# Kernel optimization log

Measured on AMD Instinct MI355X. Metric: run time of the kernel, lower is better.

Reference implementation:

```python
import jax, jax.numpy as jnp
import numpy as np

N = 50000      # nodes
E = 800000     # edges (avg degree 16)
D = 128        # hidden dim
L = 3          # message-passing layers
NU = 1         # DRew nu -> delay = max(k - nu, 0)


def setup_inputs() -> dict:
    key = jax.random.key(0)
    ks = jax.random.split(key, 6)
    x = jax.random.normal(ks[0], (N, D), dtype=jnp.float32)
    edge_index = jax.random.randint(ks[1], (2, E), 0, N)          # [2, E] (src, dst)
    edge_attr = jax.random.randint(ks[2], (E,), 1, L + 1)          # edge types in {1..L}
    scale = 1.0 / np.sqrt(D).astype(np.float32)
    Ws = jax.random.normal(ks[3], (L, D, D), dtype=jnp.float32) * scale       # mlp_s per layer
    bs = jnp.zeros((L, D), dtype=jnp.float32)
    Wk = jax.random.normal(ks[4], (L, L, D, D), dtype=jnp.float32) * scale    # mlp_k, padded; layer t uses k=1..t+1
    bk = jnp.zeros((L, L, D), dtype=jnp.float32)
    eps = jnp.zeros((L,), dtype=jnp.float32)
    return dict(x=x, edge_index=edge_index, edge_attr=edge_attr,
                Ws=Ws, bs=bs, Wk=Wk, bk=bk, eps=eps)


def reference(x, edge_index, edge_attr, Ws, bs, Wk, bk, eps):
    src, dst = edge_index[0], edge_index[1]
    xs = [x]
    for t in range(L):
        xt = xs[-1]
        # out = (1 + eps) * mlp_s(x)
        out = (1.0 + eps[t]) * jax.nn.relu(xt @ Ws[t] + bs[t])
        for k in range(1, t + 2):
            delay = max(k - NU, 0)
            x_src = xs[t - delay]                       # delayed node features
            mask = (edge_attr == k).astype(xt.dtype)    # edge-type mask (replaces boolean column select)
            msg = x_src[src] * mask[:, None]            # gather + mask: [E, D]
            agg = jax.ops.segment_sum(msg, dst, num_segments=N)  # scatter-add per destination
            out = out + jax.nn.relu(agg @ Wk[t, k - 1] + bk[t, k - 1])  # mlp_k(k)
        # gin_nn_post is an empty Sequential -> identity; then F.relu; then residual
        h = jax.nn.relu(out)
        xs.append(xt + h)
    return xs[-1]
```

## Files before the change

### kernel.cpp

```cpp
#include <hip/hip_runtime.h>
#include <hip/hip_bf16.h>


#define NODES 50000
#define EDGES 800000
#define DIM   128
#define ND    ((long)NODES * DIM)
#define NB3   (3 * NODES)
#define NPART 4
#define PSIZE (NODES / NPART)
#define NROWP 50048
#define NBLKS ((NB3 + 255) / 256)
#define NCELL 96
#define SORTN (NCELL * NBLKS)

typedef __attribute__((ext_vector_type(8))) short  bf16x8;
typedef __attribute__((ext_vector_type(4))) float  f32x4;

#define LDS_STRIDE 136

__global__ __launch_bounds__(256) void init_kernel(
    const float* __restrict__ x, const float* __restrict__ Ws,
    const float* __restrict__ Wk, __hip_bfloat16* __restrict__ xb0,
    __hip_bfloat16* __restrict__ xb1, __hip_bfloat16* __restrict__ xb2,
    __hip_bfloat16* __restrict__ WT, int* __restrict__ cursor) {
  int b = blockIdx.x, tid = threadIdx.x;
  long i = (long)b * 256 + tid;
  if (i < ND / 4) {
    float4 v = ((const float4*)x)[i];
    union { __hip_bfloat16 h[4]; uint2 u; } pk;
    pk.h[0] = __float2bfloat16(v.x); pk.h[1] = __float2bfloat16(v.y);
    pk.h[2] = __float2bfloat16(v.z); pk.h[3] = __float2bfloat16(v.w);
    ((uint2*)xb0)[i] = pk.u;
  }
  if (b < 12) {
    const float* src = (b < 3) ? (Ws + (long)b * 16384) : (Wk + (long)(b - 3) * 16384);
    __hip_bfloat16* dst = WT + (long)b * 16384;
    for (int idx = tid; idx < 16384; idx += 256) {
      int k = idx >> 7, n = idx & 127;
      dst[n * 128 + k] = __float2bfloat16(src[idx]);
    }
  }
  if (b >= 12 && b < 12 + NBLKS) {
    int g = (b - 12) * 256 + tid;
    if (g < NB3) cursor[g] = 0;
  }
  if (b == 599 && tid < DIM) {
    xb0[(long)NODES * DIM + tid] = __float2bfloat16(0.f);
    xb1[(long)NODES * DIM + tid] = __float2bfloat16(0.f);
    xb2[(long)NODES * DIM + tid] = __float2bfloat16(0.f);
  }
}

__global__ __launch_bounds__(256) void hist_kernel(
    const int* __restrict__ ei, const int* __restrict__ attr,
    int* __restrict__ counts, int E) {
  int e = blockIdx.x * 256 + threadIdx.x;
  if (e >= E) return;
  atomicAdd(&counts[ei[E + e] * 3 + (attr[e] - 1)], 1);
}

__global__ __launch_bounds__(256) void scan_a_kernel(
    const int* __restrict__ counts, int* __restrict__ partial,
    int* __restrict__ blocksums, int n) {
  __shared__ int tmp[256];
  int gid = blockIdx.x * 256 + threadIdx.x;
  int v = (gid < n) ? ((counts[gid] + 3) & ~3) : 0;
  tmp[threadIdx.x] = v;
  __syncthreads();
  for (int off = 1; off < 256; off <<= 1) {
    int t = (threadIdx.x >= off) ? tmp[threadIdx.x - off] : 0;
    __syncthreads();
    tmp[threadIdx.x] += t;
    __syncthreads();
  }
  if (gid < n) partial[gid] = tmp[threadIdx.x] - v;
  if (threadIdx.x == 255) blocksums[blockIdx.x] = tmp[255];
}

__global__ __launch_bounds__(256) void scan_b_kernel(int* __restrict__ bs, int nb) {
  __shared__ int tmp[256];
  __shared__ int carry;
  if (threadIdx.x == 0) carry = 0;
  __syncthreads();
  for (int base = 0; base < nb; base += 256) {
    int gid = base + threadIdx.x;
    int v = (gid < nb) ? bs[gid] : 0;
    tmp[threadIdx.x] = v;
    __syncthreads();
    for (int off = 1; off < 256; off <<= 1) {
      int t = (threadIdx.x >= off) ? tmp[threadIdx.x - off] : 0;
      __syncthreads();
      tmp[threadIdx.x] += t;
      __syncthreads();
    }
    if (gid < nb) bs[gid] = tmp[threadIdx.x] - v + carry;
    __syncthreads();
    if (threadIdx.x == 0) carry += tmp[255];
    __syncthreads();
  }
}

__global__ __launch_bounds__(256) void scanc_bhist_kernel(
    int* __restrict__ rowptr, int* __restrict__ cursor,
    const int* __restrict__ bs, int* __restrict__ csr,
    int* __restrict__ G, int n) {
  __shared__ int h[NCELL];
  if (threadIdx.x < NCELL) h[threadIdx.x] = 0;
  __syncthreads();
  int gid = blockIdx.x * 256 + threadIdx.x;
  if (gid < n) {
    int cnt = cursor[gid];
    int pcnt = (cnt + 3) & ~3;
    int val = rowptr[gid] + bs[blockIdx.x];
    rowptr[gid] = val;
    cursor[gid] = val;
    for (int i = cnt; i < pcnt; ++i) csr[val + i] = NODES;
    if (gid == n - 1) rowptr[n] = val + pcnt;
    int c = pcnt >> 2; if (c > 31) c = 31;
    int km1 = gid - (gid / 3) * 3;
    atomicAdd(&h[km1 * 32 + (31 - c)], 1);
  }
  __syncthreads();
  if (threadIdx.x < NCELL) G[threadIdx.x * NBLKS + blockIdx.x] = h[threadIdx.x];
}

__global__ __launch_bounds__(256) void fill_kernel(
    const int* __restrict__ ei, const int* __restrict__ attr,
    int* __restrict__ cursor, int* __restrict__ csr_src, int E) {
  int p = blockIdx.x & (NPART - 1);
  int chunk = blockIdx.x >> 2;
  int e = chunk * 256 + threadIdx.x;
  if (e >= E) return;
  int d = ei[E + e];
  int lo = p * PSIZE;
  if (d < lo || d >= lo + PSIZE) return;
  int pos = atomicAdd(&cursor[d * 3 + (attr[e] - 1)], 1);
  csr_src[pos] = ei[e];
}

__global__ __launch_bounds__(256) void fscan_a_kernel(
    const int* __restrict__ in, int* __restrict__ partial,
    int* __restrict__ blocksums, int n) {
  __shared__ int tmp[256];
  int gid = blockIdx.x * 256 + threadIdx.x;
  int v = (gid < n) ? in[gid] : 0;
  tmp[threadIdx.x] = v;
  __syncthreads();
  for (int off = 1; off < 256; off <<= 1) {
    int t = (threadIdx.x >= off) ? tmp[threadIdx.x - off] : 0;
    __syncthreads();
    tmp[threadIdx.x] += t;
    __syncthreads();
  }
  if (gid < n) partial[gid] = tmp[threadIdx.x] - v;
  if (threadIdx.x == 255) blocksums[blockIdx.x] = tmp[255];
}

__global__ __launch_bounds__(256) void bfill_kernel(
    const int* __restrict__ rowptr, const int* __restrict__ G,
    const int* __restrict__ bsum2, int* __restrict__ wl) {
  __shared__ int base[NCELL];
  if (threadIdx.x < NCELL) {
    int gidx = threadIdx.x * NBLKS + blockIdx.x;
    base[threadIdx.x] = G[gidx] + bsum2[gidx >> 8];
  }
  __syncthreads();
  int b = blockIdx.x * 256 + threadIdx.x;
  if (b >= NB3) return;
  int pcnt = rowptr[b + 1] - rowptr[b];
  int c = pcnt >> 2; if (c > 31) c = 31;
  int km1 = b - (b / 3) * 3;
  int pos = atomicAdd(&base[km1 * 32 + (31 - c)], 1);
  wl[pos] = b;
}

__global__ __launch_bounds__(256, 6) void gather_kernel(
    const __hip_bfloat16* __restrict__ src,
    const int* __restrict__ rowptr, const int* __restrict__ csr,
    const int* __restrict__ wl,
    __hip_bfloat16* __restrict__ ag0, __hip_bfloat16* __restrict__ ag1,
    __hip_bfloat16* __restrict__ ag2, int nwork) {
  int group = (blockIdx.x * 256 + threadIdx.x) >> 4;
  int lane16 = threadIdx.x & 15;
  if (group >= nwork) return;
  int b = wl[group];
  int d = b / 3;
  int km1 = b - d * 3;
  __hip_bfloat16* ag = (km1 == 0) ? ag0 : ((km1 == 1) ? ag1 : ag2);
  int beg = rowptr[b], end = rowptr[b + 1];
  float a0 = 0.f, a1 = 0.f, a2 = 0.f, a3 = 0.f,
        a4 = 0.f, a5 = 0.f, a6 = 0.f, a7 = 0.f;
  for (int base = beg; base < end; base += 16) {
    int idxv = csr[base + lane16];
    int cnt = end - base; if (cnt > 16) cnt = 16;
    for (int j = 0; j < cnt; j += 4) {
      int q0 = __shfl(idxv, j + 0, 16);
      int q1 = __shfl(idxv, j + 1, 16);
      int q2 = __shfl(idxv, j + 2, 16);
      int q3 = __shfl(idxv, j + 3, 16);
      uint4 v0 = *(const uint4*)(src + (long)q0 * DIM + lane16 * 8);
      uint4 v1 = *(const uint4*)(src + (long)q1 * DIM + lane16 * 8);
      uint4 v2 = *(const uint4*)(src + (long)q2 * DIM + lane16 * 8);
      uint4 v3 = *(const uint4*)(src + (long)q3 * DIM + lane16 * 8);
      a0 += __uint_as_float(v0.x << 16) + __uint_as_float(v1.x << 16)
          + __uint_as_float(v2.x << 16) + __uint_as_float(v3.x << 16);
      a1 += __uint_as_float(v0.x & 0xffff0000u) + __uint_as_float(v1.x & 0xffff0000u)
          + __uint_as_float(v2.x & 0xffff0000u) + __uint_as_float(v3.x & 0xffff0000u);
      a2 += __uint_as_float(v0.y << 16) + __uint_as_float(v1.y << 16)
          + __uint_as_float(v2.y << 16) + __uint_as_float(v3.y << 16);
      a3 += __uint_as_float(v0.y & 0xffff0000u) + __uint_as_float(v1.y & 0xffff0000u)
          + __uint_as_float(v2.y & 0xffff0000u) + __uint_as_float(v3.y & 0xffff0000u);
      a4 += __uint_as_float(v0.z << 16) + __uint_as_float(v1.z << 16)
          + __uint_as_float(v2.z << 16) + __uint_as_float(v3.z << 16);
      a5 += __uint_as_float(v0.z & 0xffff0000u) + __uint_as_float(v1.z & 0xffff0000u)
          + __uint_as_float(v2.z & 0xffff0000u) + __uint_as_float(v3.z & 0xffff0000u);
      a6 += __uint_as_float(v0.w << 16) + __uint_as_float(v1.w << 16)
          + __uint_as_float(v2.w << 16) + __uint_as_float(v3.w << 16);
      a7 += __uint_as_float(v0.w & 0xffff0000u) + __uint_as_float(v1.w & 0xffff0000u)
          + __uint_as_float(v2.w & 0xffff0000u) + __uint_as_float(v3.w & 0xffff0000u);
    }
  }
  union { __hip_bfloat16 h[8]; uint4 u; } pk;
  pk.h[0] = __float2bfloat16(a0); pk.h[1] = __float2bfloat16(a1);
  pk.h[2] = __float2bfloat16(a2); pk.h[3] = __float2bfloat16(a3);
  pk.h[4] = __float2bfloat16(a4); pk.h[5] = __float2bfloat16(a5);
  pk.h[6] = __float2bfloat16(a6); pk.h[7] = __float2bfloat16(a7);
  *(uint4*)(ag + (long)d * DIM + lane16 * 8) = pk.u;
}

__global__ __launch_bounds__(256, 4) void lgemm_kernel(
    const __hip_bfloat16* __restrict__ xbSelf,
    const __hip_bfloat16* __restrict__ ag0,
    const __hip_bfloat16* __restrict__ ag1,
    const __hip_bfloat16* __restrict__ ag2,
    const __hip_bfloat16* __restrict__ WT,
    const float* __restrict__ bs_t,
    const float* __restrict__ bk_t,
    const float* __restrict__ epsp,
    __hip_bfloat16* __restrict__ xnb,
    float* __restrict__ xn,
    int t) {
  __shared__ __hip_bfloat16 b_lds[128 * LDS_STRIDE];

  int tid = threadIdx.x;
  long row0 = (long)blockIdx.x * 64;
  int wave = tid >> 6, lane = tid & 63;
  int l15 = lane & 15, q = lane >> 4;
  long arow = row0 + wave * 16 + l15;

  const __hip_bfloat16* Asrc[4] = {xbSelf, ag0, ag1, ag2};
  f32x4 out[8];

  for (int p = 0; p <= t + 1; ++p) {
    if (p > 0) __syncthreads();
    const __hip_bfloat16* Am = Asrc[p];
    uint4 af[4];
#pragma unroll
    for (int k0i = 0; k0i < 4; ++k0i)
      af[k0i] = *(const uint4*)(Am + arow * DIM + k0i * 32 + 8 * q);
    const __hip_bfloat16* W = (p == 0) ? (WT + (long)t * 16384)
                                       : (WT + (long)(3 + t * 3 + (p - 1)) * 16384);
    {
      const uint4* bq = (const uint4*)W;
#pragma unroll
      for (int i = 0; i < 8; ++i) {
        int idx = tid + 256 * i;
        int n = idx >> 4, k8 = idx & 15;
        uint4 v = bq[idx];
        *(uint4*)(b_lds + n * LDS_STRIDE + k8 * 8) = v;
      }
    }
    __syncthreads();

    f32x4 acc[8] = {};
#pragma unroll
    for (int k0i = 0; k0i < 4; ++k0i) {
      bf16x8 a = __builtin_bit_cast(bf16x8, af[k0i]);
#pragma unroll
      for (int j = 0; j < 8; ++j) {
        bf16x8 bfr = *(const bf16x8*)(b_lds + (16 * j + l15) * LDS_STRIDE + k0i * 32 + 8 * q);
        acc[j] = __builtin_amdgcn_mfma_f32_16x16x32_bf16(a, bfr, acc[j], 0, 0, 0);
      }
    }
    if (p == 0) {
      float sc = 1.0f + *epsp;
#pragma unroll
      for (int j = 0; j < 8; ++j) {
        float b = bs_t[16 * j + l15];
#pragma unroll
        for (int r = 0; r < 4; ++r) out[j][r] = sc * fmaxf(acc[j][r] + b, 0.f);
      }
    } else {
      const float* bb = bk_t + (p - 1) * 128;
#pragma unroll
      for (int j = 0; j < 8; ++j) {
        float b = bb[16 * j + l15];
#pragma unroll
        for (int r = 0; r < 4; ++r) out[j][r] += fmaxf(acc[j][r] + b, 0.f);
      }
    }
  }

  long rbase = row0 + wave * 16 + q * 4;
  bool fin = (xn != nullptr);
#pragma unroll
  for (int j = 0; j < 8; ++j) {
    int col = 16 * j + l15;
#pragma unroll
    for (int r = 0; r < 4; ++r) {
      long grow = rbase + r;
      if (grow < NODES) {
        float res = __bfloat162float(xbSelf[grow * DIM + col]);
        float v = res + fmaxf(out[j][r], 0.f);
        if (fin) xn[grow * DIM + col] = v;
        else     xnb[grow * DIM + col] = __float2bfloat16(v);
      }
    }
  }
}

extern "C" void kernel_launch(void* const* d_in, const int* in_sizes, int n_in,
                              void* d_out, int out_size, void* d_ws, size_t ws_size,
                              hipStream_t stream) {
  const float* x    = (const float*)d_in[0];
  const int*   ei   = (const int*)d_in[1];
  const int*   attr = (const int*)d_in[2];
  const float* Ws   = (const float*)d_in[3];
  const float* bs   = (const float*)d_in[4];
  const float* Wk   = (const float*)d_in[5];
  const float* bk   = (const float*)d_in[6];
  const float* eps  = (const float*)d_in[7];
  float* out = (float*)d_out;

  char* ws = (char*)d_ws;
  size_t off = 0;
  auto alloc = [&](size_t bytes) { char* p = ws + off; off += (bytes + 255) & ~(size_t)255; return p; };
  const size_t ROWB = (size_t)NROWP * DIM * 2;
  __hip_bfloat16* xb0  = (__hip_bfloat16*)alloc(ROWB);
  __hip_bfloat16* xb1  = (__hip_bfloat16*)alloc(ROWB);
  __hip_bfloat16* xb2  = (__hip_bfloat16*)alloc(ROWB);
  __hip_bfloat16* agA0 = (__hip_bfloat16*)alloc(ROWB);
  __hip_bfloat16* agA1 = (__hip_bfloat16*)alloc(ROWB);
  __hip_bfloat16* agA2 = (__hip_bfloat16*)alloc(ROWB);
  __hip_bfloat16* agB0 = (__hip_bfloat16*)alloc(ROWB);
  __hip_bfloat16* agB1 = (__hip_bfloat16*)alloc(ROWB);
  __hip_bfloat16* agC0 = (__hip_bfloat16*)alloc(ROWB);
  __hip_bfloat16* WT   = (__hip_bfloat16*)alloc(12 * 16384 * 2);
  int* cursor    = (int*)alloc((size_t)NB3 * 4);
  int* rowptr    = (int*)alloc((size_t)(NB3 + 1) * 4);
  int* blocksums = (int*)alloc(1024 * 4);
  int* G         = (int*)alloc((size_t)SORTN * 4);
  int* bsum2     = (int*)alloc(1024 * 4);
  int* wl        = (int*)alloc((size_t)NB3 * 4);
  int* csr_src   = (int*)alloc((size_t)(EDGES + 4 * NB3 + 16) * 4);

  int egrid  = (EDGES + 255) / 256;
  int igrid  = (int)(ND / 4 / 256);
  int fgrid  = (SORTN + 255) / 256;

  hipLaunchKernelGGL(init_kernel, dim3(igrid), dim3(256), 0, stream,
                     x, Ws, Wk, xb0, xb1, xb2, WT, cursor);
  hipLaunchKernelGGL(hist_kernel, dim3(egrid), dim3(256), 0, stream, ei, attr, cursor, EDGES);
  hipLaunchKernelGGL(scan_a_kernel, dim3(NBLKS), dim3(256), 0, stream, cursor, rowptr, blocksums, NB3);
  hipLaunchKernelGGL(scan_b_kernel, dim3(1), dim3(256), 0, stream, blocksums, NBLKS);
  hipLaunchKernelGGL(scanc_bhist_kernel, dim3(NBLKS), dim3(256), 0, stream,
                     rowptr, cursor, blocksums, csr_src, G, NB3);
  hipLaunchKernelGGL(fill_kernel, dim3(egrid * NPART), dim3(256), 0, stream, ei, attr, cursor, csr_src, EDGES);
  hipLaunchKernelGGL(fscan_a_kernel, dim3(fgrid), dim3(256), 0, stream, G, G, bsum2, SORTN);
  hipLaunchKernelGGL(scan_b_kernel, dim3(1), dim3(256), 0, stream, bsum2, fgrid);
  hipLaunchKernelGGL(bfill_kernel, dim3(NBLKS), dim3(256), 0, stream, rowptr, G, bsum2, wl);

  int ggrid = (NODES + 63) / 64;
  auto glaunch = [&](int nwork, const __hip_bfloat16* src, __hip_bfloat16* a0,
                     __hip_bfloat16* a1, __hip_bfloat16* a2) {
    int blocks = (nwork * 16 + 255) / 256;
    hipLaunchKernelGGL(gather_kernel, dim3(blocks), dim3(256), 0, stream,
                       src, rowptr, csr_src, wl, a0, a1, a2, nwork);
  };

  glaunch(3 * NODES, xb0, agA0, agA1, agA2);
  hipLaunchKernelGGL(lgemm_kernel, dim3(ggrid), dim3(256), 0, stream,
                     xb0, agA0, agA0, agA0, WT, bs + 0, bk + 0, eps + 0,
                     xb1, (float*)nullptr, 0);
  glaunch(2 * NODES, xb1, agB0, agB1, agB1);
  hipLaunchKernelGGL(lgemm_kernel, dim3(ggrid), dim3(256), 0, stream,
                     xb1, agB0, agA1, agA1, WT, bs + 128, bk + 3 * 128, eps + 1,
                     xb2, (float*)nullptr, 1);
  glaunch(NODES, xb2, agC0, agC0, agC0);
  hipLaunchKernelGGL(lgemm_kernel, dim3(ggrid), dim3(256), 0, stream,
                     xb2, agC0, agB1, agA2, WT, bs + 256, bk + 6 * 128, eps + 2,
                     (__hip_bfloat16*)nullptr, out, 2);
}
```

Measured before the change: 329.7 us.

## Fold single-block scans into consumer kernels and software-pipeline gather loads

Removes the two single-block scan_b launches. Each block of scanc_bhist now reduces the preceding blocksums itself, and bfill rescans bsum2 in every block. This saves serialized kernel launches and a one-block bottleneck, at the cost of redundant per-block reduction work. Separately, the gather loop is software-pipelined so the next four source rows are loaded before the current four are accumulated, which aims to hide gather latency.

```diff
diff --git a/kernel.cpp b/kernel.cpp
--- a/kernel.cpp
+++ b/kernel.cpp
@@ -13,6 +13,7 @@
 #define NBLKS ((NB3 + 255) / 256)
 #define NCELL 96
 #define SORTN (NCELL * NBLKS)
+#define FGRID ((SORTN + 255) / 256)
 
 typedef __attribute__((ext_vector_type(8))) short  bf16x8;
 typedef __attribute__((ext_vector_type(4))) float  f32x4;
@@ -78,41 +79,28 @@
   if (threadIdx.x == 255) blocksums[blockIdx.x] = tmp[255];
 }
 
-__global__ __launch_bounds__(256) void scan_b_kernel(int* __restrict__ bs, int nb) {
-  __shared__ int tmp[256];
-  __shared__ int carry;
-  if (threadIdx.x == 0) carry = 0;
-  __syncthreads();
-  for (int base = 0; base < nb; base += 256) {
-    int gid = base + threadIdx.x;
-    int v = (gid < nb) ? bs[gid] : 0;
-    tmp[threadIdx.x] = v;
-    __syncthreads();
-    for (int off = 1; off < 256; off <<= 1) {
-      int t = (threadIdx.x >= off) ? tmp[threadIdx.x - off] : 0;
-      __syncthreads();
-      tmp[threadIdx.x] += t;
-      __syncthreads();
-    }
-    if (gid < nb) bs[gid] = tmp[threadIdx.x] - v + carry;
-    __syncthreads();
-    if (threadIdx.x == 0) carry += tmp[255];
-    __syncthreads();
-  }
-}
-
 __global__ __launch_bounds__(256) void scanc_bhist_kernel(
     int* __restrict__ rowptr, int* __restrict__ cursor,
-    const int* __restrict__ bs, int* __restrict__ csr,
+    const int* __restrict__ blocksums, int* __restrict__ csr,
     int* __restrict__ G, int n) {
   __shared__ int h[NCELL];
-  if (threadIdx.x < NCELL) h[threadIdx.x] = 0;
-  __syncthreads();
-  int gid = blockIdx.x * 256 + threadIdx.x;
+  __shared__ int red[256];
+  int tid = threadIdx.x;
+  int partial = 0;
+  for (int i = tid; i < blockIdx.x; i += 256) partial += blocksums[i];
+  red[tid] = partial;
+  if (tid < NCELL) h[tid] = 0;
+  __syncthreads();
+  for (int off = 128; off > 0; off >>= 1) {
+    if (tid < off) red[tid] += red[tid + off];
+    __syncthreads();
+  }
+  int bsoff = red[0];
+  int gid = blockIdx.x * 256 + tid;
   if (gid < n) {
     int cnt = cursor[gid];
     int pcnt = (cnt + 3) & ~3;
-    int val = rowptr[gid] + bs[blockIdx.x];
+    int val = rowptr[gid] + bsoff;
     rowptr[gid] = val;
     cursor[gid] = val;
     for (int i = cnt; i < pcnt; ++i) csr[val + i] = NODES;
@@ -122,7 +110,7 @@
     atomicAdd(&h[km1 * 32 + (31 - c)], 1);
   }
   __syncthreads();
-  if (threadIdx.x < NCELL) G[threadIdx.x * NBLKS + blockIdx.x] = h[threadIdx.x];
+  if (tid < NCELL) G[tid * NBLKS + blockIdx.x] = h[tid];
 }
 
 __global__ __launch_bounds__(256) void fill_kernel(
@@ -159,14 +147,29 @@
 
 __global__ __launch_bounds__(256) void bfill_kernel(
     const int* __restrict__ rowptr, const int* __restrict__ G,
-    const int* __restrict__ bsum2, int* __restrict__ wl) {
+    const int* __restrict__ bsum2, int* __restrict__ wl, int nb2) {
   __shared__ int base[NCELL];
-  if (threadIdx.x < NCELL) {
-    int gidx = threadIdx.x * NBLKS + blockIdx.x;
-    base[threadIdx.x] = G[gidx] + bsum2[gidx >> 8];
-  }
-  __syncthreads();
-  int b = blockIdx.x * 256 + threadIdx.x;
+  __shared__ int ps[256];
+  int tid = threadIdx.x;
+  int v = (tid < nb2) ? bsum2[tid] : 0;
+  ps[tid] = v;
+  __syncthreads();
+  for (int off = 1; off < 256; off <<= 1) {
+    int t = (tid >= off) ? ps[tid - off] : 0;
+    __syncthreads();
+    ps[tid] += t;
+    __syncthreads();
+  }
+  int incl = ps[tid];
+  __syncthreads();
+  ps[tid] = incl - v;
+  __syncthreads();
+  if (tid < NCELL) {
+    int gidx = tid * NBLKS + blockIdx.x;
+    base[tid] = G[gidx] + ps[gidx >> 8];
+  }
+  __syncthreads();
+  int b = blockIdx.x * 256 + tid;
   if (b >= NB3) return;
   int pcnt = rowptr[b + 1] - rowptr[b];
   int c = pcnt >> 2; if (c > 31) c = 31;
@@ -194,31 +197,42 @@
   for (int base = beg; base < end; base += 16) {
     int idxv = csr[base + lane16];
     int cnt = end - base; if (cnt > 16) cnt = 16;
+    int q0 = __shfl(idxv, 0, 16);
+    int q1 = __shfl(idxv, 1, 16);
+    int q2 = __shfl(idxv, 2, 16);
+    int q3 = __shfl(idxv, 3, 16);
+    uint4 v0 = *(const uint4*)(src + (long)q0 * DIM + lane16 * 8);
+    uint4 v1 = *(const uint4*)(src + (long)q1 * DIM + lane16 * 8);
+    uint4 v2 = *(const uint4*)(src + (long)q2 * DIM + lane16 * 8);
+    uint4 v3 = *(const uint4*)(src + (long)q3 * DIM + lane16 * 8);
     for (int j = 0; j < cnt; j += 4) {
-      int q0 = __shfl(idxv, j + 0, 16);
-      int q1 = __shfl(idxv, j + 1, 16);
-      int q2 = __shfl(idxv, j + 2, 16);
-      int q3 = __shfl(idxv, j + 3, 16);
-      uint4 v0 = *(const uint4*)(src + (long)q0 * DIM + lane16 * 8);
-      uint4 v1 = *(const uint4*)(src + (long)q1 * DIM + lane16 * 8);
-      uint4 v2 = *(const uint4*)(src + (long)q2 * DIM + lane16 * 8);
-      uint4 v3 = *(const uint4*)(src + (long)q3 * DIM + lane16 * 8);
-      a0 += __uint_as_float(v0.x << 16) + __uint_as_float(v1.x << 16)
-          + __uint_as_float(v2.x << 16) + __uint_as_float(v3.x << 16);
-      a1 += __uint_as_float(v0.x & 0xffff0000u) + __uint_as_float(v1.x & 0xffff0000u)
-          + __uint_as_float(v2.x & 0xffff0000u) + __uint_as_float(v3.x & 0xffff0000u);
-      a2 += __uint_as_float(v0.y << 16) + __uint_as_float(v1.y << 16)
-          + __uint_as_float(v2.y << 16) + __uint_as_float(v3.y << 16);
-      a3 += __uint_as_float(v0.y & 0xffff0000u) + __uint_as_float(v1.y & 0xffff0000u)
-          + __uint_as_float(v2.y & 0xffff0000u) + __uint_as_float(v3.y & 0xffff0000u);
-      a4 += __uint_as_float(v0.z << 16) + __uint_as_float(v1.z << 16)
-          + __uint_as_float(v2.z << 16) + __uint_as_float(v3.z << 16);
-      a5 += __uint_as_float(v0.z & 0xffff0000u) + __uint_as_float(v1.z & 0xffff0000u)
-          + __uint_as_float(v2.z & 0xffff0000u) + __uint_as_float(v3.z & 0xffff0000u);
-      a6 += __uint_as_float(v0.w << 16) + __uint_as_float(v1.w << 16)
-          + __uint_as_float(v2.w << 16) + __uint_as_float(v3.w << 16);
-      a7 += __uint_as_float(v0.w & 0xffff0000u) + __uint_as_float(v1.w & 0xffff0000u)
-          + __uint_as_float(v2.w & 0xffff0000u) + __uint_as_float(v3.w & 0xffff0000u);
+      uint4 c0 = v0, c1 = v1, c2 = v2, c3 = v3;
+      if (j + 4 < cnt) {
+        q0 = __shfl(idxv, j + 4, 16);
+        q1 = __shfl(idxv, j + 5, 16);
+        q2 = __shfl(idxv, j + 6, 16);
+        q3 = __shfl(idxv, j + 7, 16);
+        v0 = *(const uint4*)(src + (long)q0 * DIM + lane16 * 8);
+        v1 = *(const uint4*)(src + (long)q1 * DIM + lane16 * 8);
+        v2 = *(const uint4*)(src + (long)q2 * DIM + lane16 * 8);
+        v3 = *(const uint4*)(src + (long)q3 * DIM + lane16 * 8);
+      }
+      a0 += __uint_as_float(c0.x << 16) + __uint_as_float(c1.x << 16)
+          + __uint_as_float(c2.x << 16) + __uint_as_float(c3.x << 16);
+      a1 += __uint_as_float(c0.x & 0xffff0000u) + __uint_as_float(c1.x & 0xffff0000u)
+          + __uint_as_float(c2.x & 0xffff0000u) + __uint_as_float(c3.x & 0xffff0000u);
+      a2 += __uint_as_float(c0.y << 16) + __uint_as_float(c1.y << 16)
+          + __uint_as_float(c2.y << 16) + __uint_as_float(c3.y << 16);
+      a3 += __uint_as_float(c0.y & 0xffff0000u) + __uint_as_float(c1.y & 0xffff0000u)
+          + __uint_as_float(c2.y & 0xffff0000u) + __uint_as_float(c3.y & 0xffff0000u);
+      a4 += __uint_as_float(c0.z << 16) + __uint_as_float(c1.z << 16)
+          + __uint_as_float(c2.z << 16) + __uint_as_float(c3.z << 16);
+      a5 += __uint_as_float(c0.z & 0xffff0000u) + __uint_as_float(c1.z & 0xffff0000u)
+          + __uint_as_float(c2.z & 0xffff0000u) + __uint_as_float(c3.z & 0xffff0000u);
+      a6 += __uint_as_float(c0.w << 16) + __uint_as_float(c1.w << 16)
+          + __uint_as_float(c2.w << 16) + __uint_as_float(c3.w << 16);
+      a7 += __uint_as_float(c0.w & 0xffff0000u) + __uint_as_float(c1.w & 0xffff0000u)
+          + __uint_as_float(c2.w & 0xffff0000u) + __uint_as_float(c3.w & 0xffff0000u);
     }
   }
   union { __hip_bfloat16 h[8]; uint4 u; } pk;
@@ -357,19 +371,16 @@
 
   int egrid  = (EDGES + 255) / 256;
   int igrid  = (int)(ND / 4 / 256);
-  int fgrid  = (SORTN + 255) / 256;
 
   hipLaunchKernelGGL(init_kernel, dim3(igrid), dim3(256), 0, stream,
                      x, Ws, Wk, xb0, xb1, xb2, WT, cursor);
   hipLaunchKernelGGL(hist_kernel, dim3(egrid), dim3(256), 0, stream, ei, attr, cursor, EDGES);
   hipLaunchKernelGGL(scan_a_kernel, dim3(NBLKS), dim3(256), 0, stream, cursor, rowptr, blocksums, NB3);
-  hipLaunchKernelGGL(scan_b_kernel, dim3(1), dim3(256), 0, stream, blocksums, NBLKS);
   hipLaunchKernelGGL(scanc_bhist_kernel, dim3(NBLKS), dim3(256), 0, stream,
                      rowptr, cursor, blocksums, csr_src, G, NB3);
   hipLaunchKernelGGL(fill_kernel, dim3(egrid * NPART), dim3(256), 0, stream, ei, attr, cursor, csr_src, EDGES);
-  hipLaunchKernelGGL(fscan_a_kernel, dim3(fgrid), dim3(256), 0, stream, G, G, bsum2, SORTN);
-  hipLaunchKernelGGL(scan_b_kernel, dim3(1), dim3(256), 0, stream, bsum2, fgrid);
-  hipLaunchKernelGGL(bfill_kernel, dim3(NBLKS), dim3(256), 0, stream, rowptr, G, bsum2, wl);
+  hipLaunchKernelGGL(fscan_a_kernel, dim3(FGRID), dim3(256), 0, stream, G, G, bsum2, SORTN);
+  hipLaunchKernelGGL(bfill_kernel, dim3(NBLKS), dim3(256), 0, stream, rowptr, G, bsum2, wl, FGRID);
 
   int ggrid = (NODES + 63) / 64;
   auto glaunch = [&](int nwork, const __hip_bfloat16* src, __hip_bfloat16* a0,
```

Result: no change. 324.1 us (-1.7%).
